# Performance work log

Hardware: AMD Instinct MI355X
Metric: run time of the kernel (lower is better)

The kernel has to match this reference:

```python
import jax, jax.numpy as jnp
import numpy as np

EPS = 1e-12

def setup_inputs() -> dict:
    key = jax.random.key(0)
    ks = jax.random.split(key, 7)
    bs, seq, d_in, d_out = 8, 2048, 4096, 4096
    n_tasks, n_splits, n_skills, rank = 64, 1, 8, 16
    return {
        "x": jax.random.normal(ks[0], (bs, seq, d_in), dtype=jnp.float32),
        "weight": jax.random.normal(ks[1], (d_out, d_in), dtype=jnp.float32) * 0.02,
        "bias": jax.random.normal(ks[2], (d_out,), dtype=jnp.float32) * 0.02,
        "module_logits": jax.random.normal(ks[3], (n_tasks, n_splits * n_skills), dtype=jnp.float32) * 0.001,
        "lora_a": jax.random.normal(ks[4], (n_splits, n_skills, d_in // n_splits, rank), dtype=jnp.float32) * 0.02,
        "lora_b": jax.random.normal(ks[5], (n_splits, n_skills, rank, d_out // n_splits), dtype=jnp.float32) * 0.02,
        "task_ids": jax.random.randint(ks[6], (bs,), 0, n_tasks, dtype=jnp.int64),
    }

def reference(x, weight, bias, module_logits, lora_a, lora_b, task_ids):
    # Eval-mode PolytroponSelector: sigmoid then sum-normalize per split.
    n_splits, n_skills, _, rank = lora_a.shape
    bs = x.shape[0]
    mw = jax.nn.sigmoid(module_logits[task_ids]).reshape(bs, n_splits, n_skills)
    mw = mw / (mw.sum(axis=-1, keepdims=True) + EPS)
    # Mix per-skill LoRA factors: A [bs, in, rank], B [bs, rank, out]
    A = jnp.einsum('bqs,qsdr->bqdr', mw, lora_a).reshape(bs, -1, rank)
    B = jnp.einsum('bqs,qsrd->bqrd', mw, lora_b)
    B = jnp.transpose(B, (0, 2, 1, 3)).reshape(bs, rank, -1)
    # Low-rank adapter path: (x @ A) @ B / rank
    adapter = jnp.einsum('btr,bro->bto', jnp.einsum('bti,bir->btr', x, A), B) / rank
    # Base linear + adapter
    return jnp.einsum('bti,oi->bto', x, weight) + bias + adapter
```

## Files before the change

kernel.cpp:

```cpp
#include <hip/hip_runtime.h>
#include <hip/hip_bf16.h>
#include <cstdint>
#include <cstddef>

typedef __attribute__((ext_vector_type(4))) float floatx4;
typedef __attribute__((ext_vector_type(8))) __bf16 bf16x8;

#define BS 8
#define SEQ 2048
#define M_TOT 16384
#define DK 4096
#define DN 4096
#define NSK 8
#define RANK 16

__device__ __forceinline__ unsigned short f2bf(float f) {
  union { __hip_bfloat16 h; unsigned short u; } v;
  v.h = __float2bfloat16(f);
  return v.u;
}

__device__ __forceinline__ void async16(const void* g, void* l) {
  __builtin_amdgcn_global_load_lds(
      (const __attribute__((address_space(1))) unsigned int*)g,
      (__attribute__((address_space(3))) unsigned int*)l, 16, 0, 0);
}

__global__ void prep_mw_kernel(const float* __restrict__ logits,
                               const void* __restrict__ task_raw,
                               float* __restrict__ mw) {
  const int* t32 = (const int*)task_raw;
  bool is64 = true;
#pragma unroll
  for (int b = 0; b < BS; ++b)
    if (t32[2 * b + 1] != 0) is64 = false;
  int tid = threadIdx.x;
  int b = tid >> 3, s = tid & 7;
  int task = is64 ? t32[2 * b] : t32[b];
  float lg = logits[task * NSK + s];
  float sg = 1.0f / (1.0f + expf(-lg));
  float sum = sg;
  sum += __shfl_xor(sum, 1);
  sum += __shfl_xor(sum, 2);
  sum += __shfl_xor(sum, 4);
  mw[tid] = sg / (sum + 1e-12f);
}

__global__ __launch_bounds__(256) void prep_a_kernel(
    const float* __restrict__ lora_a, const float* __restrict__ mw,
    unsigned short* __restrict__ a_bft) {
  int b = blockIdx.y;
  int d = blockIdx.x * 256 + threadIdx.x;
  float w[NSK];
#pragma unroll
  for (int s = 0; s < NSK; ++s) w[s] = mw[b * NSK + s];
  float acc[RANK];
#pragma unroll
  for (int r = 0; r < RANK; ++r) acc[r] = 0.f;
  for (int s = 0; s < NSK; ++s) {
    const float4* p = (const float4*)&lora_a[((size_t)s * DK + d) * RANK];
#pragma unroll
    for (int q = 0; q < 4; ++q) {
      float4 v = p[q];
      acc[q * 4 + 0] += w[s] * v.x;
      acc[q * 4 + 1] += w[s] * v.y;
      acc[q * 4 + 2] += w[s] * v.z;
      acc[q * 4 + 3] += w[s] * v.w;
    }
  }
#pragma unroll
  for (int r = 0; r < RANK; ++r)
    a_bft[((size_t)b * RANK + r) * DK + d] = f2bf(acc[r]);
}

__global__ __launch_bounds__(256) void prep_b_kernel(
    const float* __restrict__ lora_b, const float* __restrict__ mw,
    unsigned short* __restrict__ baug) {
  int b = blockIdx.y;
  int n = blockIdx.x * 256 + threadIdx.x;
  float w[NSK];
#pragma unroll
  for (int s = 0; s < NSK; ++s) w[s] = mw[b * NSK + s];
  unsigned short ov[32];
#pragma unroll
  for (int r = 0; r < RANK; ++r) {
    float acc = 0.f;
#pragma unroll
    for (int s = 0; s < NSK; ++s)
      acc += w[s] * lora_b[((size_t)s * RANK + r) * DN + n];
    ov[r] = f2bf(acc * 0.0625f);
  }
#pragma unroll
  for (int r = RANK; r < 32; ++r) ov[r] = 0;
  uint4* dst = (uint4*)&baug[((size_t)b * DN + n) * 32];
  const uint4* sv = (const uint4*)ov;
  dst[0] = sv[0]; dst[1] = sv[1]; dst[2] = sv[2]; dst[3] = sv[3];
}

__global__ __launch_bounds__(256) void conv_f32_to_bf16(
    const float* __restrict__ src, unsigned short* __restrict__ dst,
    long long n4) {
  long long stride = (long long)gridDim.x * 256;
  for (long long i = (long long)blockIdx.x * 256 + threadIdx.x; i < n4; i += stride) {
    float4 v = ((const float4*)src)[i];
    ushort4 o;
    o.x = f2bf(v.x); o.y = f2bf(v.y); o.z = f2bf(v.z); o.w = f2bf(v.w);
    ((ushort4*)dst)[i] = o;
  }
}

__global__ __launch_bounds__(256) void t_gemm_kernel(
    const unsigned short* __restrict__ xb, const unsigned short* __restrict__ abft,
    float* __restrict__ t_f32) {
  const int wave = threadIdx.x >> 6;
  const int lane = threadIdx.x & 63;
  const int mtile = blockIdx.x * 4 + wave;
  const int row0 = mtile * 16;
  const int b = row0 >> 11;
  const int k0 = blockIdx.y * 1024;
  const int fr = lane & 15;
  const int fq = (lane >> 4) * 8;
  const unsigned short* pa = xb + (size_t)(row0 + fr) * DK + fq + k0;
  const unsigned short* pb = abft + ((size_t)b * RANK + fr) * DK + fq + k0;
  floatx4 acc = {0.f, 0.f, 0.f, 0.f};
  for (int k = 0; k < 1024; k += 32) {
    bf16x8 av = *(const bf16x8*)(pa + k);
    bf16x8 bv = *(const bf16x8*)(pb + k);
    acc = __builtin_amdgcn_mfma_f32_16x16x32_bf16(av, bv, acc, 0, 0, 0);
  }
  const int col = lane & 15;
  const int rowq = (lane >> 4) * 4;
#pragma unroll
  for (int j = 0; j < 4; ++j)
    atomicAdd(&t_f32[(size_t)(row0 + rowq + j) * RANK + col], acc[j]);
}

__global__ __launch_bounds__(256) void t_final_kernel(
    const float* __restrict__ t_f32, unsigned short* __restrict__ taug) {
  int i = blockIdx.x * 256 + threadIdx.x;
  int row = i >> 4, r = i & 15;
  taug[(size_t)row * 32 + r] = f2bf(t_f32[i]);
  taug[(size_t)row * 32 + 16 + r] = 0;
}

__global__ __launch_bounds__(512, 2) void main_gemm(
    const unsigned short* __restrict__ xb, const unsigned short* __restrict__ wb,
    const unsigned short* __restrict__ taug, const unsigned short* __restrict__ baug,
    const float* __restrict__ bias, float* __restrict__ out) {
  __shared__ __align__(1024) unsigned short lds[65536];

  const int tid = threadIdx.x;
  const int wave = tid >> 6;
  const int lane = tid & 63;
  const int wm = wave >> 2;
  const int wn = wave & 3;
  const int fr = lane & 15;
  const int fq = (lane >> 4) << 3;
  const int swz = (lane & 12) << 1;

  const int orig = blockIdx.x;
  const int swb = (orig & 7) * 128 + (orig >> 3);
  const int tile_m = swb >> 4;
  const int tile_n = swb & 15;
  const int m0 = tile_m * 256;
  const int n0 = tile_n * 256;
  const int batch = tile_m >> 3;

  const int l16 = lane << 4;
  const int o = l16 ^ ((l16 & 512) >> 4) ^ ((l16 & 256) >> 4);
  const int rin = o >> 6;
  const int k2 = (o & 63) >> 1;
  const int s0 = wave * 2, s1 = s0 + 1;
  const unsigned short* aS0 = xb + (size_t)(m0 + (s0 & 7) * 16 + rin) * DK + (s0 >> 3) * 32 + k2;
  const unsigned short* aS1 = xb + (size_t)(m0 + (s1 & 7) * 16 + rin) * DK + (s1 >> 3) * 32 + k2;
  const unsigned short* bS0 = wb + (size_t)(n0 + (s0 & 7) * 16 + rin) * DK + (s0 >> 3) * 32 + k2;
  const unsigned short* bS1 = wb + (size_t)(n0 + (s1 & 7) * 16 + rin) * DK + (s1 >> 3) * 32 + k2;

#define STG_A(d, h, kt) do {                                                        \
    async16(aS0 + (((size_t)(h)) << 19) + ((size_t)(kt) << 6),                      \
            &lds[(d) * 32768 + (h) * 8192 + s0 * 512]);                             \
    async16(aS1 + (((size_t)(h)) << 19) + ((size_t)(kt) << 6),                      \
            &lds[(d) * 32768 + (h) * 8192 + s1 * 512]);                             \
  } while (0)
#define STG_B(d, h, kt) do {                                                        \
    async16(bS0 + (((size_t)(h)) << 19) + ((size_t)(kt) << 6),                      \
            &lds[(d) * 32768 + 16384 + (h) * 8192 + s0 * 512]);                     \
    async16(bS1 + (((size_t)(h)) << 19) + ((size_t)(kt) << 6),                      \
            &lds[(d) * 32768 + 16384 + (h) * 8192 + s1 * 512]);                     \
  } while (0)

#define RD_A(d, t, ks)                                                              \
  (*(const bf16x8*)&lds[(((d) * 32768) + wm * 8192 + (ks) * 4096 +                  \
                         ((t) * 16 + fr) * 32 + fq) ^ swz])
#define RD_B(d, u, ks)                                                              \
  (*(const bf16x8*)&lds[(((d) * 32768) + 16384 + (wn >> 1) * 8192 + (ks) * 4096 +   \
                         ((wn & 1) * 64 + (u) * 16 + fr) * 32 + fq) ^ swz])

  floatx4 acc[8][4];
#pragma unroll
  for (int t = 0; t < 8; ++t)
#pragma unroll
    for (int u = 0; u < 4; ++u) acc[t][u] = (floatx4){0.f, 0.f, 0.f, 0.f};

  bf16x8 a[4][2];
  bf16x8 b0[2][2];
  bf16x8 b1[2][2];

  STG_A(0, 0, 0); STG_A(0, 1, 0); STG_B(0, 0, 0); STG_B(0, 1, 0);
  STG_A(1, 0, 1); STG_A(1, 1, 1); STG_B(1, 0, 1);
  asm volatile("s_waitcnt vmcnt(6)" ::: "memory");
  __builtin_amdgcn_s_barrier();

#define TILE(d, kt) do {                                                            \
                      \
    _Pragma("unroll")                                                               \
    for (int t = 0; t < 4; ++t) { a[t][0] = RD_A(d, t, 0); a[t][1] = RD_A(d, t, 1); } \
    _Pragma("unroll")                                                               \
    for (int u = 0; u < 2; ++u) { b0[u][0] = RD_B(d, u, 0); b0[u][1] = RD_B(d, u, 1); } \
    if ((kt) + 1 < 64) STG_B(1 - (d), 1, (kt) + 1);                                 \
    __builtin_amdgcn_s_barrier();                                                   \
    asm volatile("s_waitcnt lgkmcnt(0)" ::: "memory");                              \
    __builtin_amdgcn_s_setprio(1);                                                  \
    _Pragma("unroll")                                                               \
    for (int t = 0; t < 4; ++t)                                                     \
      _Pragma("unroll")                                                             \
      for (int u = 0; u < 2; ++u) {                                                 \
        acc[t][u] = __builtin_amdgcn_mfma_f32_16x16x32_bf16(a[t][0], b0[u][0], acc[t][u], 0, 0, 0); \
        acc[t][u] = __builtin_amdgcn_mfma_f32_16x16x32_bf16(a[t][1], b0[u][1], acc[t][u], 0, 0, 0); \
      }                                                                             \
    __builtin_amdgcn_s_setprio(0);                                                  \
    __builtin_amdgcn_s_barrier();                                                   \
                                             \
    _Pragma("unroll")                                                               \
    for (int u = 0; u < 2; ++u) { b1[u][0] = RD_B(d, u + 2, 0); b1[u][1] = RD_B(d, u + 2, 1); } \
    __builtin_amdgcn_s_barrier();                                                   \
    asm volatile("s_waitcnt lgkmcnt(0)" ::: "memory");                              \
    __builtin_amdgcn_s_setprio(1);                                                  \
    _Pragma("unroll")                                                               \
    for (int t = 0; t < 4; ++t)                                                     \
      _Pragma("unroll")                                                             \
      for (int u = 0; u < 2; ++u) {                                                 \
        acc[t][u + 2] = __builtin_amdgcn_mfma_f32_16x16x32_bf16(a[t][0], b1[u][0], acc[t][u + 2], 0, 0, 0); \
        acc[t][u + 2] = __builtin_amdgcn_mfma_f32_16x16x32_bf16(a[t][1], b1[u][1], acc[t][u + 2], 0, 0, 0); \
      }                                                                             \
    __builtin_amdgcn_s_setprio(0);                                                  \
    __builtin_amdgcn_s_barrier();                                                   \
                                             \
    _Pragma("unroll")                                                               \
    for (int t = 0; t < 4; ++t) { a[t][0] = RD_A(d, t + 4, 0); a[t][1] = RD_A(d, t + 4, 1); } \
    __builtin_amdgcn_s_barrier();                                                   \
    asm volatile("s_waitcnt lgkmcnt(0)" ::: "memory");                              \
    __builtin_amdgcn_s_setprio(1);                                                  \
    _Pragma("unroll")                                                               \
    for (int t = 0; t < 4; ++t)                                                     \
      _Pragma("unroll")                                                             \
      for (int u = 0; u < 2; ++u) {                                                 \
        acc[t + 4][u] = __builtin_amdgcn_mfma_f32_16x16x32_bf16(a[t][0], b0[u][0], acc[t + 4][u], 0, 0, 0); \
        acc[t + 4][u] = __builtin_amdgcn_mfma_f32_16x16x32_bf16(a[t][1], b0[u][1], acc[t + 4][u], 0, 0, 0); \
      }                                                                             \
    __builtin_amdgcn_s_setprio(0);                                                  \
    __builtin_amdgcn_s_barrier();                                                   \
         \
        \
    if ((kt) + 2 < 64) {                                                            \
      STG_A(d, 0, (kt) + 2); STG_A(d, 1, (kt) + 2); STG_B(d, 0, (kt) + 2);          \
      asm volatile("s_waitcnt vmcnt(6)" ::: "memory");                              \
    } else {                                                                        \
      asm volatile("s_waitcnt vmcnt(0)" ::: "memory");                              \
    }                                                                               \
    __builtin_amdgcn_s_barrier();                                                   \
    __builtin_amdgcn_s_setprio(1);                                                  \
    _Pragma("unroll")                                                               \
    for (int t = 0; t < 4; ++t)                                                     \
      _Pragma("unroll")                                                             \
      for (int u = 0; u < 2; ++u) {                                                 \
        acc[t + 4][u + 2] = __builtin_amdgcn_mfma_f32_16x16x32_bf16(a[t][0], b1[u][0], acc[t + 4][u + 2], 0, 0, 0); \
        acc[t + 4][u + 2] = __builtin_amdgcn_mfma_f32_16x16x32_bf16(a[t][1], b1[u][1], acc[t + 4][u + 2], 0, 0, 0); \
      }                                                                             \
    __builtin_amdgcn_s_setprio(0);                                                  \
    __builtin_amdgcn_s_barrier();                                                   \
  } while (0)

  for (int it = 0; it < 32; ++it) {
    const int kt0 = it * 2;
    TILE(0, kt0);
    TILE(1, kt0 + 1);
  }

  {
    const unsigned short* tA = taug + (size_t)(m0 + wm * 128 + fr) * 32 + fq;
    const unsigned short* tB = baug + ((size_t)batch * DN + n0 + wn * 64 + fr) * 32 + fq;
    bf16x8 av[8], bv[4];
#pragma unroll
    for (int t = 0; t < 8; ++t) av[t] = *(const bf16x8*)(tA + (size_t)t * 512);
#pragma unroll
    for (int u = 0; u < 4; ++u) bv[u] = *(const bf16x8*)(tB + (size_t)u * 512);
#pragma unroll
    for (int t = 0; t < 8; ++t)
#pragma unroll
      for (int u = 0; u < 4; ++u)
        acc[t][u] = __builtin_amdgcn_mfma_f32_16x16x32_bf16(av[t], bv[u], acc[t][u], 0, 0, 0);
  }

  const int rowq = (lane >> 4) * 4;
#pragma unroll
  for (int u = 0; u < 4; ++u) {
    const int col = n0 + wn * 64 + u * 16 + fr;
    const float bvv = bias[col];
#pragma unroll
    for (int t = 0; t < 8; ++t) {
      float* po = out + (size_t)(m0 + wm * 128 + t * 16 + rowq) * DN + col;
#pragma unroll
      for (int j = 0; j < 4; ++j) po[(size_t)j * DN] = acc[t][u][j] + bvv;
    }
  }
#undef TILE
#undef RD_A
#undef RD_B
#undef STG_A
#undef STG_B
}

extern "C" void kernel_launch(void* const* d_in, const int* in_sizes, int n_in,
                              void* d_out, int out_size, void* d_ws, size_t ws_size,
                              hipStream_t stream) {
  (void)in_sizes; (void)n_in; (void)out_size; (void)ws_size;
  const float* x             = (const float*)d_in[0];
  const float* weight        = (const float*)d_in[1];
  const float* bias          = (const float*)d_in[2];
  const float* module_logits = (const float*)d_in[3];
  const float* lora_a        = (const float*)d_in[4];
  const float* lora_b        = (const float*)d_in[5];
  const void*  task_ids      = d_in[6];
  float* out = (float*)d_out;

  char* ws = (char*)d_ws;
  unsigned short* xb   = (unsigned short*)(ws);
  unsigned short* wb   = (unsigned short*)(ws + 134217728);
  unsigned short* taug = (unsigned short*)(ws + 167772160);
  unsigned short* baug = (unsigned short*)(ws + 168820736);
  unsigned short* abft = (unsigned short*)(ws + 170917888);
  float*          tf32 = (float*)(ws + 171966464);
  float*          mw   = (float*)(ws + 173015040);

  hipLaunchKernelGGL(prep_mw_kernel, dim3(1), dim3(64), 0, stream,
                     module_logits, task_ids, mw);
  hipLaunchKernelGGL(prep_a_kernel, dim3(16, 8), dim3(256), 0, stream,
                     lora_a, mw, abft);
  hipLaunchKernelGGL(prep_b_kernel, dim3(16, 8), dim3(256), 0, stream,
                     lora_b, mw, baug);
  hipLaunchKernelGGL(conv_f32_to_bf16, dim3(2048), dim3(256), 0, stream,
                     weight, wb, (long long)(4096LL * 4096 / 4));
  hipLaunchKernelGGL(conv_f32_to_bf16, dim3(8192), dim3(256), 0, stream,
                     x, xb, (long long)(16384LL * 4096 / 4));
  hipMemsetAsync(tf32, 0, (size_t)M_TOT * RANK * sizeof(float), stream);
  hipLaunchKernelGGL(t_gemm_kernel, dim3(256, 4), dim3(256), 0, stream,
                     xb, abft, tf32);
  hipLaunchKernelGGL(t_final_kernel, dim3(1024), dim3(256), 0, stream,
                     tf32, taug);
  hipLaunchKernelGGL(main_gemm, dim3(1024), dim3(512), 0, stream,
                     xb, wb, taug, baug, bias, out);
}
```

Measured before the change: 1.179 ms.

## Switch LDS tile layout to row-major 64-element rows with XOR swizzle

```diff
diff --git a/kernel.cpp b/kernel.cpp
--- a/kernel.cpp
+++ b/kernel.cpp
@@ -156,7 +156,6 @@
   const int wn = wave & 3;
   const int fr = lane & 15;
   const int fq = (lane >> 4) << 3;
-  const int swz = (lane & 12) << 1;
 
   const int orig = blockIdx.x;
   const int swb = (orig & 7) * 128 + (orig >> 3);
@@ -166,35 +165,34 @@
   const int n0 = tile_n * 256;
   const int batch = tile_m >> 3;
 
-  const int l16 = lane << 4;
-  const int o = l16 ^ ((l16 & 512) >> 4) ^ ((l16 & 256) >> 4);
-  const int rin = o >> 6;
-  const int k2 = (o & 63) >> 1;
-  const int s0 = wave * 2, s1 = s0 + 1;
-  const unsigned short* aS0 = xb + (size_t)(m0 + (s0 & 7) * 16 + rin) * DK + (s0 >> 3) * 32 + k2;
-  const unsigned short* aS1 = xb + (size_t)(m0 + (s1 & 7) * 16 + rin) * DK + (s1 >> 3) * 32 + k2;
-  const unsigned short* bS0 = wb + (size_t)(n0 + (s0 & 7) * 16 + rin) * DK + (s0 >> 3) * 32 + k2;
-  const unsigned short* bS1 = wb + (size_t)(n0 + (s1 & 7) * 16 + rin) * DK + (s1 >> 3) * 32 + k2;
+  const int laneoff = (lane >> 3) * DK + (((lane & 7) ^ (lane >> 3)) << 3);
+  const unsigned short* aSrc = xb + (size_t)(m0 + 16 * wave) * DK + laneoff;
+  const unsigned short* bSrc = wb + (size_t)(n0 + 16 * wave) * DK + laneoff;
 
 #define STG_A(d, h, kt) do {                                                        \
-    async16(aS0 + (((size_t)(h)) << 19) + ((size_t)(kt) << 6),                      \
-            &lds[(d) * 32768 + (h) * 8192 + s0 * 512]);                             \
-    async16(aS1 + (((size_t)(h)) << 19) + ((size_t)(kt) << 6),                      \
-            &lds[(d) * 32768 + (h) * 8192 + s1 * 512]);                             \
+    async16(aSrc + (size_t)(h) * (128 * DK) + ((size_t)(kt) << 6),                  \
+            &lds[(d) * 32768 + (h) * 8192 + wave * 1024]);                          \
+    async16(aSrc + (size_t)(h) * (128 * DK) + 8 * DK + ((size_t)(kt) << 6),         \
+            &lds[(d) * 32768 + (h) * 8192 + wave * 1024 + 512]);                    \
   } while (0)
 #define STG_B(d, h, kt) do {                                                        \
-    async16(bS0 + (((size_t)(h)) << 19) + ((size_t)(kt) << 6),                      \
-            &lds[(d) * 32768 + 16384 + (h) * 8192 + s0 * 512]);                     \
-    async16(bS1 + (((size_t)(h)) << 19) + ((size_t)(kt) << 6),                      \
-            &lds[(d) * 32768 + 16384 + (h) * 8192 + s1 * 512]);                     \
+    async16(bSrc + (size_t)(h) * (128 * DK) + ((size_t)(kt) << 6),                  \
+            &lds[(d) * 32768 + 16384 + (h) * 8192 + wave * 1024]);                  \
+    async16(bSrc + (size_t)(h) * (128 * DK) + 8 * DK + ((size_t)(kt) << 6),         \
+            &lds[(d) * 32768 + 16384 + (h) * 8192 + wave * 1024 + 512]);            \
   } while (0)
 
+  const int colb0 = fq ^ ((fr & 7) << 3);
+  const int colb1 = colb0 ^ 32;
+  const int aRd0 = wm * 8192 + fr * 64 + colb0;
+  const int aRd1 = wm * 8192 + fr * 64 + colb1;
+  const int bRd0 = 16384 + wn * 4096 + fr * 64 + colb0;
+  const int bRd1 = 16384 + wn * 4096 + fr * 64 + colb1;
+
 #define RD_A(d, t, ks)                                                              \
-  (*(const bf16x8*)&lds[(((d) * 32768) + wm * 8192 + (ks) * 4096 +                  \
-                         ((t) * 16 + fr) * 32 + fq) ^ swz])
+  (*(const bf16x8*)&lds[(d) * 32768 + ((ks) ? aRd1 : aRd0) + (t) * 1024])
 #define RD_B(d, u, ks)                                                              \
-  (*(const bf16x8*)&lds[(((d) * 32768) + 16384 + (wn >> 1) * 8192 + (ks) * 4096 +   \
-                         ((wn & 1) * 64 + (u) * 16 + fr) * 32 + fq) ^ swz])
+  (*(const bf16x8*)&lds[(d) * 32768 + ((ks) ? bRd1 : bRd0) + (u) * 1024])
 
   floatx4 acc[8][4];
 #pragma unroll
```

Measured after the change: 1.001 ms. -15.1%, faster.
